# Performance work log

Hardware: AMD Instinct MI355X
Metric: run time of the kernel (lower is better)

The kernel has to match this reference:

```python
import jax, jax.numpy as jnp
import numpy as np

D = 4096
B = 8192
MEM = 50
TWO_PI = 2.0 * np.pi
PHI = 1.618033


def setup_inputs() -> dict:
    key = jax.random.key(0)
    ks = jax.random.split(key, 10)
    inp = {
        "x": jax.random.normal(ks[0], (B, D), dtype=jnp.float32),
        "crystal_state": jax.random.normal(ks[1], (D,), dtype=jnp.float32) * 0.05,
        "phase_memory": jax.random.uniform(ks[2], (MEM,), dtype=jnp.float32) * TWO_PI,
        "coherence_momentum": jnp.ones((1,), dtype=jnp.float32) * 0.9,
        "crystal_weights": jax.random.normal(ks[3], (D,), dtype=jnp.float32) * 0.05,
        "Wf": jax.random.normal(ks[4], (D,), dtype=jnp.float32) * 0.02,
        "bf": jnp.zeros((1,), dtype=jnp.float32),
        "Wamp": jax.random.normal(ks[5], (D, D), dtype=jnp.float32) * 0.02,
        "bamp": jnp.zeros((D,), dtype=jnp.float32),
        "Wtemp": jax.random.normal(ks[6], (D, D), dtype=jnp.float32) * 0.02,
        "btemp": jnp.zeros((D,), dtype=jnp.float32),
        "Wgate": jax.random.normal(ks[7], (D, D), dtype=jnp.float32) * 0.02,
        "bgate": jnp.zeros((D,), dtype=jnp.float32),
        "time_step": 100,
    }
    return inp


def reference(x, crystal_state, phase_memory, coherence_momentum, crystal_weights,
              Wf, bf, Wamp, bamp, Wtemp, btemp, Wgate, bgate, time_step):
    sg = jax.lax.stop_gradient
    ts = time_step + 1  # python int, time_step increments at call start

    # --- detached dynamics (torch runs these under no_grad / on detached input) ---
    mean_x = sg(x).mean(0)  # [D]
    freq_adj = jax.nn.sigmoid(jnp.dot(Wf, mean_x) + bf[0])
    actual_frequency = 1.618033 * (1.0 + freq_adj * 0.2)  # PHASE_COUPLING=0.2
    t = ts / 100.0
    primary_phase = jnp.mod(TWO_PI * t * actual_frequency, TWO_PI)
    secondary_phase = jnp.mod(primary_phase / PHI, TWO_PI)
    crystal_oscillation = 0.3 * (jnp.sin(primary_phase) + 0.3 * jnp.cos(secondary_phase))

    enhanced_weights = crystal_weights * (1.0 + jnp.tanh(Wamp @ mean_x + bamp))
    new_crystal_state = sg(0.98 * crystal_state + 0.02 * crystal_oscillation * enhanced_weights)

    pm = jnp.roll(phase_memory, 1).at[0].set(primary_phase)
    # ts = 101 > 10 and MEM > 2: coherence branch (static python control flow)
    s1, s2 = pm[::2], pm[1::2]  # 25 each
    phase_periods = s1 - s2
    period_consistency = jnp.clip(1.0 - jnp.std(phase_periods, ddof=1) / TWO_PI, 0.0, 1.0)
    crystal_coherence = 0.9 * (1.0 + period_consistency * 0.2)
    stability_factor = min(ts / 1000.0, 1.0)
    coherence = crystal_coherence * (1.0 + stability_factor * 0.3)
    new_momentum = 0.98 * coherence_momentum[0] + 0.02 * coherence
    coherence = sg(jnp.clip(new_momentum, 0.9 * 0.8, 0.9 * 1.5))

    # --- differentiable enhancement path ---
    time_factor = 1.0 + min(ts / 5000.0, 0.5)
    enhancement_factor = coherence * 1.2 * time_factor  # TEMPORAL_BOOST=1.2
    crystal_enhancement = jax.nn.sigmoid(x @ Wgate.T + bgate)  # [B,D]
    enhanced_input = x + crystal_enhancement * new_crystal_state[None, :] * enhancement_factor * 0.3
    temporal_features = jnp.tanh(enhanced_input @ Wtemp.T + btemp)
    temporal_boost = 1.0 + coherence * 0.2 * time_factor
    final_enhanced_input = enhanced_input + temporal_features * temporal_boost * 0.15
    return final_enhanced_input
```

## Files before the change

### kernel.cpp

```cpp
#include <hip/hip_runtime.h>

typedef unsigned short u16;
typedef __attribute__((ext_vector_type(8))) short bf16x8;
typedef __attribute__((ext_vector_type(4))) float f32x4;

#define GK 4096
#define GN 4096
#define BDIM 4096
#define BROWS 8192

__device__ __forceinline__ u16 f2b(float f) {
    union { float f; unsigned u; } c; c.f = f;
    unsigned u = c.u;
    return (u16)((u + 0x7FFFu + ((u >> 16) & 1u)) >> 16);
}
__device__ __forceinline__ float b2f(u16 h) {
    union { unsigned u; float f; } c; c.u = ((unsigned)h) << 16;
    return c.f;
}
__device__ __forceinline__ void gload16(const void* g, void* l) {
    __builtin_amdgcn_global_load_lds((const __attribute__((address_space(1))) void*)g,
                                     (__attribute__((address_space(3))) void*)l, 16, 0, 0);
}

__global__ void k_cvt_colsum(const float* __restrict__ x, u16* __restrict__ xb,
                             float* __restrict__ colsum) {
    const int tid  = threadIdx.x;
    const int c4   = blockIdx.x * 64 + (tid & 63);
    const int rowg = tid >> 6;
    const int r0   = blockIdx.y * 128;
    const float4* x4 = (const float4*)x;
    float sx = 0.f, sy = 0.f, sz = 0.f, sw = 0.f;
    for (int i = 0; i < 32; ++i) {
        int row = r0 + i * 4 + rowg;
        float4 v = x4[(size_t)row * 1024 + c4];
        sx += v.x; sy += v.y; sz += v.z; sw += v.w;
        ushort4 o; o.x = f2b(v.x); o.y = f2b(v.y); o.z = f2b(v.z); o.w = f2b(v.w);
        *(ushort4*)(xb + (size_t)row * BDIM + c4 * 4) = o;
    }
    __shared__ float red[256][4];
    red[tid][0] = sx; red[tid][1] = sy; red[tid][2] = sz; red[tid][3] = sw;
    __syncthreads();
    if (tid < 64) {
        for (int j = 64; j < 256; j += 64) {
            sx += red[tid + j][0]; sy += red[tid + j][1];
            sz += red[tid + j][2]; sw += red[tid + j][3];
        }
        int c = blockIdx.x * 64 + tid;
        atomicAdd(&colsum[c * 4 + 0], sx);
        atomicAdd(&colsum[c * 4 + 1], sy);
        atomicAdd(&colsum[c * 4 + 2], sz);
        atomicAdd(&colsum[c * 4 + 3], sw);
    }
}

__global__ void k_cvt2(const float4* __restrict__ a, ushort4* __restrict__ ao,
                       const float4* __restrict__ b, ushort4* __restrict__ bo) {
    int i = blockIdx.x * 256 + threadIdx.x;
    const float4* in;  ushort4* out;
    if (i < 4194304) { in = a; out = ao; }
    else             { in = b; out = bo; i -= 4194304; }
    float4 v = in[i];
    ushort4 o; o.x = f2b(v.x); o.y = f2b(v.y); o.z = f2b(v.z); o.w = f2b(v.w);
    out[i] = o;
}

__global__ void k_scalars(const float* __restrict__ colsum, const float* __restrict__ Wf,
                          const float* __restrict__ bfp, const float* __restrict__ pmem,
                          const float* __restrict__ cmom, const int* __restrict__ tstep,
                          float* __restrict__ sc) {
    const int tid = threadIdx.x;
    float s = 0.f;
    for (int i = tid; i < BDIM; i += 256) s += Wf[i] * colsum[i];
    __shared__ float red[256];
    red[tid] = s; __syncthreads();
    for (int off = 128; off > 0; off >>= 1) {
        if (tid < off) red[tid] += red[tid + off];
        __syncthreads();
    }
    if (tid == 0) {
        const float TP = 6.283185307179586f;
        float mdot = red[0] * (1.f / (float)BROWS) + bfp[0];
        float fa = 1.f / (1.f + expf(-mdot));
        int ts = tstep[0] + 1;
        float t = (float)ts / 100.f;
        float af = 1.618033f * (1.f + fa * 0.2f);
        float pp = fmodf(TP * t * af, TP);
        float sp = fmodf(pp / 1.618033f, TP);
        float co = 0.3f * (sinf(pp) + 0.3f * cosf(sp));
        float d[25];
        d[0] = pp - pmem[0];
        for (int j = 1; j < 25; ++j) d[j] = pmem[2 * j - 1] - pmem[2 * j];
        float m = 0.f;
        for (int j = 0; j < 25; ++j) m += d[j];
        m *= (1.f / 25.f);
        float var = 0.f;
        for (int j = 0; j < 25; ++j) { float e = d[j] - m; var += e * e; }
        var *= (1.f / 24.f);
        float sd = sqrtf(var);
        float pc = fminf(fmaxf(1.f - sd / TP, 0.f), 1.f);
        float cc = 0.9f * (1.f + pc * 0.2f);
        float stab = fminf((float)ts / 1000.f, 1.f);
        float coh1 = cc * (1.f + stab * 0.3f);
        float nm = 0.98f * cmom[0] + 0.02f * coh1;
        float coh = fminf(fmaxf(nm, 0.72f), 1.35f);
        float tf = 1.f + fminf((float)ts / 5000.f, 0.5f);
        sc[0] = co;
        sc[1] = coh * 1.2f * tf * 0.3f;
        sc[2] = (1.f + coh * 0.2f * tf) * 0.15f;
    }
}

__global__ void k_csef(const float* __restrict__ Wamp, const float* __restrict__ colsum,
                       const float* __restrict__ bamp, const float* __restrict__ cw,
                       const float* __restrict__ cstate, const float* __restrict__ sc,
                       float* __restrict__ csef) {
    const int row = blockIdx.x, tid = threadIdx.x;
    const float4* w4 = (const float4*)(Wamp + (size_t)row * BDIM);
    const float4* m4 = (const float4*)colsum;
    float s = 0.f;
    for (int i = tid; i < 1024; i += 256) {
        float4 w = w4[i], m = m4[i];
        s += w.x * m.x + w.y * m.y + w.z * m.z + w.w * m.w;
    }
    __shared__ float red[256];
    red[tid] = s; __syncthreads();
    for (int off = 128; off > 0; off >>= 1) {
        if (tid < off) red[tid] += red[tid + off];
        __syncthreads();
    }
    if (tid == 0) {
        float v = red[0] * (1.f / (float)BROWS) + bamp[row];
        float ew = cw[row] * (1.f + tanhf(v));
        float cs = 0.98f * cstate[row] + 0.02f * sc[0] * ew;
        csef[row] = cs * sc[1];
    }
}

template <int MODE>
__global__ __launch_bounds__(256) void gemm_bt(
    const u16* __restrict__ A, const u16* __restrict__ Bm,
    const float* __restrict__ xf, const float* __restrict__ bias,
    const float* __restrict__ csef, const float* __restrict__ sc,
    u16* __restrict__ outb, float* __restrict__ outf) {
    __shared__ u16 As[128 * 64];
    __shared__ u16 Bs[128 * 64];

    const int tid = threadIdx.x;
    const int lane = tid & 63;
    const int wave = tid >> 6;
    const int waveM = wave >> 1;
    const int waveN = wave & 1;
    const int bm0 = blockIdx.y * 128;
    const int bn0 = blockIdx.x * 128;

    const u16* ag[4]; const u16* bg[4];
    u16* la[4]; u16* lb[4];
    {
        const int lr = lane >> 3;
        const int lc = lane & 7;
        const int gcol = (lc ^ lr) * 8;
#pragma unroll
        for (int i = 0; i < 4; ++i) {
            int sseg = wave * 4 + i;
            int r = sseg * 8 + lr;
            ag[i] = A + (size_t)(bm0 + r) * GK + gcol;
            bg[i] = Bm + (size_t)(bn0 + r) * GK + gcol;
            la[i] = &As[sseg * 512];
            lb[i] = &Bs[sseg * 512];
        }
    }

    f32x4 acc[4][4] = {};
    const int lm = lane & 15;
    const int quad = lane >> 4;
    const int arow = waveM * 64 + lm;
    const int brow = waveN * 64 + lm;
    const int rsw = lm & 7;

    for (int k0 = 0; k0 < GK; k0 += 64) {
#pragma unroll
        for (int i = 0; i < 4; ++i) {
            gload16(ag[i] + k0, la[i]);
            gload16(bg[i] + k0, lb[i]);
        }
        __syncthreads();
#pragma unroll
        for (int kk = 0; kk < 2; ++kk) {
            const int pch = ((kk * 4 + quad) ^ rsw) * 8;
            bf16x8 a[4], b[4];
#pragma unroll
            for (int mi = 0; mi < 4; ++mi)
                a[mi] = *(const bf16x8*)&As[(arow + mi * 16) * 64 + pch];
#pragma unroll
            for (int ni = 0; ni < 4; ++ni)
                b[ni] = *(const bf16x8*)&Bs[(brow + ni * 16) * 64 + pch];
#pragma unroll
            for (int mi = 0; mi < 4; ++mi)
#pragma unroll
                for (int ni = 0; ni < 4; ++ni)
                    acc[mi][ni] = __builtin_amdgcn_mfma_f32_16x16x32_bf16(
                        a[mi], b[ni], acc[mi][ni], 0, 0, 0);
        }
        __syncthreads();
    }

    const int col0 = bn0 + waveN * 64 + lm;
    const int row0 = bm0 + waveM * 64 + quad * 4;
    const float tb15 = (MODE == 2) ? sc[2] : 0.f;
#pragma unroll
    for (int mi = 0; mi < 4; ++mi) {
#pragma unroll
        for (int r = 0; r < 4; ++r) {
            const int row = row0 + mi * 16 + r;
#pragma unroll
            for (int ni = 0; ni < 4; ++ni) {
                const int col = col0 + ni * 16;
                const float v = acc[mi][ni][r];
                const size_t idx = (size_t)row * GN + col;
                if (MODE == 1) {
                    float vb = v + bias[col];
                    vb = fminf(fmaxf(vb, -30.f), 30.f);
                    float sg = 1.f / (1.f + __expf(-vb));
                    float e = xf[idx] + csef[col] * sg;
                    outb[idx] = f2b(e);
                } else {
                    float vb = v + bias[col];
                    vb = fminf(fmaxf(vb, -15.f), 15.f);
                    float e2 = __expf(2.f * vb);
                    float th = (e2 - 1.f) / (e2 + 1.f);
                    outf[idx] = b2f(A[idx]) + th * tb15;
                }
            }
        }
    }
}

extern "C" void kernel_launch(void* const* d_in, const int* in_sizes, int n_in,
                              void* d_out, int out_size, void* d_ws, size_t ws_size,
                              hipStream_t stream) {
    const float* x      = (const float*)d_in[0];
    const float* cstate = (const float*)d_in[1];
    const float* pmem   = (const float*)d_in[2];
    const float* cmom   = (const float*)d_in[3];
    const float* cw     = (const float*)d_in[4];
    const float* Wf     = (const float*)d_in[5];
    const float* bfp    = (const float*)d_in[6];
    const float* Wamp   = (const float*)d_in[7];
    const float* bamp   = (const float*)d_in[8];
    const float* Wtemp  = (const float*)d_in[9];
    const float* btemp  = (const float*)d_in[10];
    const float* Wgate  = (const float*)d_in[11];
    const float* bgate  = (const float*)d_in[12];
    const int*   tstep  = (const int*)d_in[13];
    float* out = (float*)d_out;

    char* ws = (char*)d_ws;
    u16* x_bf   = (u16*)ws;  ws += (size_t)BROWS * BDIM * 2;
    u16* wg_bf  = (u16*)ws;  ws += (size_t)BDIM * BDIM * 2;
    u16* wt_bf  = (u16*)ws;  ws += (size_t)BDIM * BDIM * 2;
    u16* enh_bf = (u16*)ws;  ws += (size_t)BROWS * BDIM * 2;
    float* colsum = (float*)ws; ws += BDIM * 4;
    float* csef   = (float*)ws; ws += BDIM * 4;
    float* sc     = (float*)ws; ws += 256;

    hipMemsetAsync(colsum, 0, BDIM * sizeof(float), stream);
    k_cvt_colsum<<<dim3(16, 64), 256, 0, stream>>>(x, x_bf, colsum);
    k_cvt2<<<32768, 256, 0, stream>>>((const float4*)Wgate, (ushort4*)wg_bf,
                                      (const float4*)Wtemp, (ushort4*)wt_bf);
    k_scalars<<<1, 256, 0, stream>>>(colsum, Wf, bfp, pmem, cmom, tstep, sc);
    k_csef<<<4096, 256, 0, stream>>>(Wamp, colsum, bamp, cw, cstate, sc, csef);
    gemm_bt<1><<<dim3(32, 64), 256, 0, stream>>>(x_bf, wg_bf, x, bgate, csef, sc, enh_bf, nullptr);
    gemm_bt<2><<<dim3(32, 64), 256, 0, stream>>>(enh_bf, wt_bf, nullptr, btemp, nullptr, sc, nullptr, out);
}
```

Baseline: 1.093 ms.

## Replace GEMM with 256x256 double-buffered, phase-interleaved MFMA pipeline

Replaces the 128x128 single-buffered bf16 GEMM with a 256x256 tile kernel of 512 threads. It double-buffers the LDS K-slices and splits each K-step into four phases that interleave async global-to-LDS loads with MFMA blocks, using explicit vmcnt waits, barriers and setprio. It also swizzles the block index for L2 locality and hoists the bias and csef loads out of the epilogue loop. The goal is to hide global load latency, raise arithmetic intensity per LDS byte, and get closer to peak matrix throughput. In exchange it uses much more LDS and registers, and the hand-written synchronisation is fragile.

```diff
diff --git a/kernel.cpp b/kernel.cpp
--- a/kernel.cpp
+++ b/kernel.cpp
@@ -137,95 +137,215 @@
     }
 }
 
+template <bool STAGE, int W1, int W2>
+__device__ __forceinline__ void gemm_tile(
+    const u16* __restrict__ Ab, const u16* __restrict__ Bb,
+    u16* __restrict__ An, u16* __restrict__ Bn, int ks,
+    const u16* const (&aAg)[4], const u16* const (&bBg)[4],
+    const int (&aLd)[4], const int (&bLd)[4],
+    int apos, int bpos, int c0, int c1,
+    bf16x8 (&a)[4][2], bf16x8 (&q0)[2][2], bf16x8 (&q1)[2][2],
+    f32x4 (&acc)[8][4])
+{
+#pragma unroll
+    for (int f = 0; f < 4; ++f) {
+        a[f][0] = *(const bf16x8*)(Ab + apos + f * 1024 + c0);
+        a[f][1] = *(const bf16x8*)(Ab + apos + f * 1024 + c1);
+    }
+#pragma unroll
+    for (int f = 0; f < 2; ++f) {
+        q0[f][0] = *(const bf16x8*)(Bb + bpos + f * 1024 + c0);
+        q0[f][1] = *(const bf16x8*)(Bb + bpos + f * 1024 + c1);
+    }
+    if constexpr (STAGE) {
+        gload16(bBg[0] + ks, Bn + bLd[0]);
+        gload16(bBg[1] + ks, Bn + bLd[1]);
+    }
+    __builtin_amdgcn_s_barrier();
+    __builtin_amdgcn_s_setprio(1);
+#pragma unroll
+    for (int mf = 0; mf < 4; ++mf)
+#pragma unroll
+        for (int nf = 0; nf < 2; ++nf) {
+            acc[mf][nf] = __builtin_amdgcn_mfma_f32_16x16x32_bf16(a[mf][0], q0[nf][0], acc[mf][nf], 0, 0, 0);
+            acc[mf][nf] = __builtin_amdgcn_mfma_f32_16x16x32_bf16(a[mf][1], q0[nf][1], acc[mf][nf], 0, 0, 0);
+        }
+    __builtin_amdgcn_s_setprio(0);
+    if constexpr (W1 == 4) asm volatile("s_waitcnt vmcnt(4)" ::: "memory");
+    else                   asm volatile("s_waitcnt vmcnt(2)" ::: "memory");
+    __builtin_amdgcn_s_barrier();
+    __builtin_amdgcn_sched_barrier(0);
+
+#pragma unroll
+    for (int f = 0; f < 2; ++f) {
+        q1[f][0] = *(const bf16x8*)(Bb + bpos + (2 + f) * 1024 + c0);
+        q1[f][1] = *(const bf16x8*)(Bb + bpos + (2 + f) * 1024 + c1);
+    }
+    if constexpr (STAGE) {
+        gload16(aAg[0] + ks, An + aLd[0]);
+        gload16(aAg[1] + ks, An + aLd[1]);
+    }
+    __builtin_amdgcn_s_barrier();
+    __builtin_amdgcn_s_setprio(1);
+#pragma unroll
+    for (int mf = 0; mf < 4; ++mf)
+#pragma unroll
+        for (int nf = 0; nf < 2; ++nf) {
+            acc[mf][2 + nf] = __builtin_amdgcn_mfma_f32_16x16x32_bf16(a[mf][0], q1[nf][0], acc[mf][2 + nf], 0, 0, 0);
+            acc[mf][2 + nf] = __builtin_amdgcn_mfma_f32_16x16x32_bf16(a[mf][1], q1[nf][1], acc[mf][2 + nf], 0, 0, 0);
+        }
+    __builtin_amdgcn_s_setprio(0);
+    if constexpr (W2 == 4) asm volatile("s_waitcnt vmcnt(4)" ::: "memory");
+    else                   asm volatile("s_waitcnt vmcnt(0)" ::: "memory");
+    __builtin_amdgcn_s_barrier();
+    __builtin_amdgcn_sched_barrier(0);
+
+#pragma unroll
+    for (int f = 0; f < 4; ++f) {
+        a[f][0] = *(const bf16x8*)(Ab + apos + (4 + f) * 1024 + c0);
+        a[f][1] = *(const bf16x8*)(Ab + apos + (4 + f) * 1024 + c1);
+    }
+    if constexpr (STAGE) {
+        gload16(bBg[2] + ks, Bn + bLd[2]);
+        gload16(bBg[3] + ks, Bn + bLd[3]);
+    }
+    __builtin_amdgcn_s_barrier();
+    __builtin_amdgcn_s_setprio(1);
+#pragma unroll
+    for (int mf = 0; mf < 4; ++mf)
+#pragma unroll
+        for (int nf = 0; nf < 2; ++nf) {
+            acc[4 + mf][nf] = __builtin_amdgcn_mfma_f32_16x16x32_bf16(a[mf][0], q0[nf][0], acc[4 + mf][nf], 0, 0, 0);
+            acc[4 + mf][nf] = __builtin_amdgcn_mfma_f32_16x16x32_bf16(a[mf][1], q0[nf][1], acc[4 + mf][nf], 0, 0, 0);
+        }
+    __builtin_amdgcn_s_setprio(0);
+    __builtin_amdgcn_s_barrier();
+    __builtin_amdgcn_sched_barrier(0);
+
+    if constexpr (STAGE) {
+        gload16(aAg[2] + ks, An + aLd[2]);
+        gload16(aAg[3] + ks, An + aLd[3]);
+    }
+    __builtin_amdgcn_s_barrier();
+    __builtin_amdgcn_s_setprio(1);
+#pragma unroll
+    for (int mf = 0; mf < 4; ++mf)
+#pragma unroll
+        for (int nf = 0; nf < 2; ++nf) {
+            acc[4 + mf][2 + nf] = __builtin_amdgcn_mfma_f32_16x16x32_bf16(a[mf][0], q1[nf][0], acc[4 + mf][2 + nf], 0, 0, 0);
+            acc[4 + mf][2 + nf] = __builtin_amdgcn_mfma_f32_16x16x32_bf16(a[mf][1], q1[nf][1], acc[4 + mf][2 + nf], 0, 0, 0);
+        }
+    __builtin_amdgcn_s_setprio(0);
+    if constexpr (STAGE) asm volatile("s_waitcnt vmcnt(4)" ::: "memory");
+    __builtin_amdgcn_s_barrier();
+    __builtin_amdgcn_sched_barrier(0);
+}
+
 template <int MODE>
-__global__ __launch_bounds__(256) void gemm_bt(
+__global__ __launch_bounds__(512, 2) void gemm256(
     const u16* __restrict__ A, const u16* __restrict__ Bm,
     const float* __restrict__ xf, const float* __restrict__ bias,
     const float* __restrict__ csef, const float* __restrict__ sc,
-    u16* __restrict__ outb, float* __restrict__ outf) {
-    __shared__ u16 As[128 * 64];
-    __shared__ u16 Bs[128 * 64];
-
-    const int tid = threadIdx.x;
+    u16* __restrict__ outb, float* __restrict__ outf)
+{
+    __shared__ u16 As[2 * 256 * 64];
+    __shared__ u16 Bs[2 * 256 * 64];
+
+    const int tid  = threadIdx.x;
     const int lane = tid & 63;
     const int wave = tid >> 6;
-    const int waveM = wave >> 1;
-    const int waveN = wave & 1;
-    const int bm0 = blockIdx.y * 128;
-    const int bn0 = blockIdx.x * 128;
-
-    const u16* ag[4]; const u16* bg[4];
-    u16* la[4]; u16* lb[4];
-    {
-        const int lr = lane >> 3;
-        const int lc = lane & 7;
-        const int gcol = (lc ^ lr) * 8;
-#pragma unroll
-        for (int i = 0; i < 4; ++i) {
-            int sseg = wave * 4 + i;
-            int r = sseg * 8 + lr;
-            ag[i] = A + (size_t)(bm0 + r) * GK + gcol;
-            bg[i] = Bm + (size_t)(bn0 + r) * GK + gcol;
-            la[i] = &As[sseg * 512];
-            lb[i] = &Bs[sseg * 512];
-        }
-    }
-
-    f32x4 acc[4][4] = {};
-    const int lm = lane & 15;
+    const int wm = wave >> 2;
+    const int wn = wave & 3;
+
+    const int bid = blockIdx.x;
+    const int swz = (bid & 7) * 64 + (bid >> 3);
+    const int bn0 = (swz >> 5) * 256;
+    const int bm0 = (swz & 31) * 256;
+
+    const int lr = lane >> 3, lc = lane & 7;
+    const int gch = (lc ^ lr) * 8;
+    const int rA = wn;
+    const int rB = wm * 2 + (wn & 1);
+    const int awin[4] = {rA, 4 + rA, 8 + rA, 12 + rA};
+    const int bwin[4] = {rB, 8 + rB, 4 + rB, 12 + rB};
+    const u16* aAg[4]; const u16* bBg[4];
+    int aLd[4], bLd[4];
+#pragma unroll
+    for (int j = 0; j < 4; ++j) {
+        aAg[j] = A  + (size_t)(bm0 + wm * 128 + awin[j] * 8 + lr) * GK + gch;
+        bBg[j] = Bm + (size_t)(bn0 + (wn >> 1) * 128 + bwin[j] * 8 + lr) * GK + gch;
+        aLd[j] = (wm * 128 + awin[j] * 8) * 64;
+        bLd[j] = ((wn >> 1) * 128 + bwin[j] * 8) * 64;
+    }
+
+    const int lm   = lane & 15;
     const int quad = lane >> 4;
-    const int arow = waveM * 64 + lm;
-    const int brow = waveN * 64 + lm;
-    const int rsw = lm & 7;
-
-    for (int k0 = 0; k0 < GK; k0 += 64) {
-#pragma unroll
-        for (int i = 0; i < 4; ++i) {
-            gload16(ag[i] + k0, la[i]);
-            gload16(bg[i] + k0, lb[i]);
-        }
-        __syncthreads();
-#pragma unroll
-        for (int kk = 0; kk < 2; ++kk) {
-            const int pch = ((kk * 4 + quad) ^ rsw) * 8;
-            bf16x8 a[4], b[4];
-#pragma unroll
-            for (int mi = 0; mi < 4; ++mi)
-                a[mi] = *(const bf16x8*)&As[(arow + mi * 16) * 64 + pch];
-#pragma unroll
-            for (int ni = 0; ni < 4; ++ni)
-                b[ni] = *(const bf16x8*)&Bs[(brow + ni * 16) * 64 + pch];
-#pragma unroll
-            for (int mi = 0; mi < 4; ++mi)
-#pragma unroll
-                for (int ni = 0; ni < 4; ++ni)
-                    acc[mi][ni] = __builtin_amdgcn_mfma_f32_16x16x32_bf16(
-                        a[mi], b[ni], acc[mi][ni], 0, 0, 0);
-        }
-        __syncthreads();
-    }
-
-    const int col0 = bn0 + waveN * 64 + lm;
-    const int row0 = bm0 + waveM * 64 + quad * 4;
+    const int rsw  = lm & 7;
+    const int apos = (wm * 128 + lm) * 64;
+    const int bpos = (wn * 64 + lm) * 64;
+    const int c0 = (quad ^ rsw) * 8;
+    const int c1 = ((4 + quad) ^ rsw) * 8;
+
+    f32x4 acc[8][4];
+#pragma unroll
+    for (int i = 0; i < 8; ++i)
+#pragma unroll
+        for (int j = 0; j < 4; ++j) acc[i][j] = (f32x4){0.f, 0.f, 0.f, 0.f};
+
+    gload16(bBg[0], Bs + bLd[0]);
+    gload16(bBg[1], Bs + bLd[1]);
+    gload16(aAg[0], As + aLd[0]);
+    gload16(aAg[1], As + aLd[1]);
+    gload16(bBg[2], Bs + bLd[2]);
+    gload16(bBg[3], Bs + bLd[3]);
+    gload16(aAg[2], As + aLd[2]);
+    gload16(aAg[3], As + aLd[3]);
+    asm volatile("s_waitcnt vmcnt(4)" ::: "memory");
+    __builtin_amdgcn_s_barrier();
+    __builtin_amdgcn_sched_barrier(0);
+
+    bf16x8 a[4][2], q0[2][2], q1[2][2];
+
+#pragma unroll 2
+    for (int T = 0; T < 63; ++T) {
+        const u16* Ab = As + ((T & 1) << 14);
+        const u16* Bb = Bs + ((T & 1) << 14);
+        u16* An = As + (((T + 1) & 1) << 14);
+        u16* Bn = Bs + (((T + 1) & 1) << 14);
+        const int ks = (T + 1) * 64;
+        gemm_tile<true, 4, 4>(Ab, Bb, An, Bn, ks, aAg, bBg, aLd, bLd,
+                              apos, bpos, c0, c1, a, q0, q1, acc);
+    }
+    gemm_tile<false, 2, 0>(As + (1 << 14), Bs + (1 << 14), As, Bs, 0,
+                           aAg, bBg, aLd, bLd, apos, bpos, c0, c1, a, q0, q1, acc);
+
+    const int col0 = bn0 + wn * 64 + lm;
+    const int row0 = bm0 + wm * 128 + quad * 4;
+    float bias_v[4], csef_v[4];
+#pragma unroll
+    for (int nf = 0; nf < 4; ++nf) {
+        bias_v[nf] = bias[col0 + nf * 16];
+        if (MODE == 1) csef_v[nf] = csef[col0 + nf * 16];
+    }
     const float tb15 = (MODE == 2) ? sc[2] : 0.f;
 #pragma unroll
-    for (int mi = 0; mi < 4; ++mi) {
+    for (int mf = 0; mf < 8; ++mf) {
 #pragma unroll
         for (int r = 0; r < 4; ++r) {
-            const int row = row0 + mi * 16 + r;
-#pragma unroll
-            for (int ni = 0; ni < 4; ++ni) {
-                const int col = col0 + ni * 16;
-                const float v = acc[mi][ni][r];
+            const int row = row0 + mf * 16 + r;
+#pragma unroll
+            for (int nf = 0; nf < 4; ++nf) {
+                const int col = col0 + nf * 16;
+                const float v = acc[mf][nf][r];
                 const size_t idx = (size_t)row * GN + col;
                 if (MODE == 1) {
-                    float vb = v + bias[col];
+                    float vb = v + bias_v[nf];
                     vb = fminf(fmaxf(vb, -30.f), 30.f);
                     float sg = 1.f / (1.f + __expf(-vb));
-                    float e = xf[idx] + csef[col] * sg;
+                    float e = xf[idx] + csef_v[nf] * sg;
                     outb[idx] = f2b(e);
                 } else {
-                    float vb = v + bias[col];
+                    float vb = v + bias_v[nf];
                     vb = fminf(fmaxf(vb, -15.f), 15.f);
                     float e2 = __expf(2.f * vb);
                     float th = (e2 - 1.f) / (e2 + 1.f);
@@ -270,6 +390,6 @@
                                       (const float4*)Wtemp, (ushort4*)wt_bf);
     k_scalars<<<1, 256, 0, stream>>>(colsum, Wf, bfp, pmem, cmom, tstep, sc);
     k_csef<<<4096, 256, 0, stream>>>(Wamp, colsum, bamp, cw, cstate, sc, csef);
-    gemm_bt<1><<<dim3(32, 64), 256, 0, stream>>>(x_bf, wg_bf, x, bgate, csef, sc, enh_bf, nullptr);
-    gemm_bt<2><<<dim3(32, 64), 256, 0, stream>>>(enh_bf, wt_bf, nullptr, btemp, nullptr, sc, nullptr, out);
-}
+    gemm256<1><<<512, 512, 0, stream>>>(x_bf, wg_bf, x, bgate, csef, sc, enh_bf, nullptr);
+    gemm256<2><<<512, 512, 0, stream>>>(enh_bf, wt_bf, nullptr, btemp, nullptr, sc, nullptr, out);
+}
```

Measured after the change: 878.4 us. -19.7%, faster.
